# Kernel tuning notes

Hardware: AMD Instinct MI355X
Metric: run time of the kernel (lower is better)

Reference implementation:

```python
import jax, jax.numpy as jnp
import numpy as np

DEPTH, BREADTH, N_HEADS = 6, 1024, 16
D_HEAD = BREADTH // N_HEADS
EPS = 1e-5


def layer_norm(x, g, b):
    m = jnp.mean(x, axis=-1, keepdims=True)
    v = jnp.mean(jnp.square(x - m), axis=-1, keepdims=True)
    return (x - m) * jax.lax.rsqrt(v + EPS) * g + b


def setup_inputs() -> dict:
    key = jax.random.key(0)
    ks = jax.random.split(key, 16)
    B, S, Dm, Dff = 4, 1024, BREADTH, 4 * BREADTH
    s = 0.02
    return {
        "x": jax.random.normal(ks[0], (B, S, Dm), dtype=jnp.float32),
        "mask": jnp.ones((B, S, S), dtype=jnp.int32),
        "wq": s * jax.random.normal(ks[1], (DEPTH, Dm, Dm), dtype=jnp.float32),
        "bq": jnp.zeros((DEPTH, Dm), dtype=jnp.float32),
        "wk": s * jax.random.normal(ks[2], (DEPTH, Dm, Dm), dtype=jnp.float32),
        "bk": jnp.zeros((DEPTH, Dm), dtype=jnp.float32),
        "wv": s * jax.random.normal(ks[3], (DEPTH, Dm, Dm), dtype=jnp.float32),
        "bv": jnp.zeros((DEPTH, Dm), dtype=jnp.float32),
        "wo": s * jax.random.normal(ks[4], (DEPTH, Dm, Dm), dtype=jnp.float32),
        "bo": jnp.zeros((DEPTH, Dm), dtype=jnp.float32),
        "w1": s * jax.random.normal(ks[5], (DEPTH, Dm, Dff), dtype=jnp.float32),
        "b1": jnp.zeros((DEPTH, Dff), dtype=jnp.float32),
        "w2": s * jax.random.normal(ks[6], (DEPTH, Dff, Dm), dtype=jnp.float32),
        "b2": jnp.zeros((DEPTH, Dm), dtype=jnp.float32),
        "ln1g": jnp.ones((DEPTH, Dm), dtype=jnp.float32),
        "ln1b": jnp.zeros((DEPTH, Dm), dtype=jnp.float32),
        "ln2g": jnp.ones((DEPTH, Dm), dtype=jnp.float32),
        "ln2b": jnp.zeros((DEPTH, Dm), dtype=jnp.float32),
        "lnfg": jnp.ones((Dm,), dtype=jnp.float32),
        "lnfb": jnp.zeros((Dm,), dtype=jnp.float32),
    }


def reference(x, mask, wq, bq, wk, bk, wv, bv, wo, bo, w1, b1, w2, b2,
              ln1g, ln1b, ln2g, ln2b, lnfg, lnfb):
    B, S, Dm = x.shape
    scale = 1.0 / jnp.sqrt(jnp.float32(D_HEAD))
    neg = jnp.float32(-1e9)
    mask_b = (mask == 0)[:, None]  # [B,1,S,S]

    def split_heads(t):  # [B,S,Dm] -> [B,H,S,d]
        return t.reshape(B, S, N_HEADS, D_HEAD).transpose(0, 2, 1, 3)

    for i in range(DEPTH):
        xn1 = layer_norm(x, ln1g[i], ln1b[i])  # attention branch input
        xn2 = layer_norm(x, ln2g[i], ln2b[i])  # FFN branch input (pre-attention, per original)

        q = split_heads(xn1 @ wq[i] + bq[i])
        k = split_heads(xn1 @ wk[i] + bk[i])
        v = split_heads(xn1 @ wv[i] + bv[i])
        scores = jnp.einsum("bhqd,bhkd->bhqk", q, k) * scale
        scores = jnp.where(mask_b, neg, scores)
        attn = jax.nn.softmax(scores, axis=-1)
        ctx = jnp.einsum("bhqk,bhkd->bhqd", attn, v)
        ctx = ctx.transpose(0, 2, 1, 3).reshape(B, S, Dm)
        x = x + (ctx @ wo[i] + bo[i])

        h = jax.nn.relu(xn2 @ w1[i] + b1[i])
        x = x + (h @ w2[i] + b2[i])

    return layer_norm(x, lnfg, lnfb)
```

## Files before the change

### kernel.cpp

```cpp
#include <hip/hip_runtime.h>
#include <hip/hip_bf16.h>
#include <stdint.h>

#define DEPTH 6
#define DM 1024
#define DFF 4096
#define NH 16
#define DH 64
#define BATCH 4
#define SEQ 1024
#define NTOK (BATCH*SEQ)
#define QKVLD 3072

using bf16x8 = __attribute__((ext_vector_type(8))) short;
using f32x4  = __attribute__((ext_vector_type(4))) float;
typedef unsigned short u16;

__device__ __forceinline__ u16 f2bf(float f) {
  union { float f; uint32_t u; } v; v.f = f;
  return (u16)((v.u + 0x7FFFu + ((v.u >> 16) & 1u)) >> 16);
}

__device__ __forceinline__ void async16(void* lds, const void* g) {
  __builtin_amdgcn_global_load_lds(
      (__attribute__((address_space(1))) void*)(unsigned long long)g,
      (__attribute__((address_space(3))) void*)(unsigned int)(unsigned long long)lds,
      16, 0, 0);
}

__global__ __launch_bounds__(256)
void prep(const float* __restrict__ wq, const float* __restrict__ wk,
          const float* __restrict__ wv, const float* __restrict__ wo,
          const float* __restrict__ w1, const float* __restrict__ w2,
          const float* __restrict__ bq, const float* __restrict__ bk,
          const float* __restrict__ bv,
          u16* __restrict__ wqkvT, u16* __restrict__ woT,
          u16* __restrict__ w1T, u16* __restrict__ w2T,
          float* __restrict__ bqkv) {
  const int bid = blockIdx.x;
  if (bid >= 12288) {
    const int t = (bid - 12288) * 256 + threadIdx.x;
    bqkv[t] = t < 1024 ? bq[t] : (t < 2048 ? bk[t - 1024] : bv[t - 2048]);
    return;
  }
  const float* w; u16* wt; int K, N, tile;
  if (bid < 3072)      { const int r = bid >> 10;
                         w = r == 0 ? wq : (r == 1 ? wk : wv);
                         wt = wqkvT + (size_t)r * 1024 * 1024; K = 1024; N = 1024; tile = bid & 1023; }
  else if (bid < 4096) { w = wo; wt = woT; K = 1024; N = 1024; tile = bid - 3072; }
  else if (bid < 8192) { w = w1; wt = w1T; K = 1024; N = 4096; tile = bid - 4096; }
  else                 { w = w2; wt = w2T; K = 4096; N = 1024; tile = bid - 8192; }
  const int ntn = N >> 5;
  const int k0 = (tile / ntn) << 5, n0 = (tile % ntn) << 5;

  __shared__ u16 t[32][33];
  const int tx = threadIdx.x & 31, ty = threadIdx.x >> 5;
  #pragma unroll
  for (int r = ty; r < 32; r += 8)
    t[r][tx] = f2bf(w[(size_t)(k0 + r) * N + n0 + tx]);
  __syncthreads();
  #pragma unroll
  for (int r = ty; r < 32; r += 8)
    wt[(size_t)(n0 + r) * K + k0 + tx] = t[tx][r];
}

__global__ __launch_bounds__(256)
void vtrans(const u16* __restrict__ qkv, u16* __restrict__ vt) {
  __shared__ u16 t[64][72];
  const int s0 = blockIdx.x * 64, c0 = blockIdx.y * 64, b = blockIdx.z;
  const int r = threadIdx.x >> 2, cq = threadIdx.x & 3;
  const u16* src = qkv + ((size_t)(b * SEQ + s0 + r)) * QKVLD + 2048 + c0 + cq * 16;
  *(bf16x8*)&t[r][cq * 16]     = *(const bf16x8*)(src);
  *(bf16x8*)&t[r][cq * 16 + 8] = *(const bf16x8*)(src + 8);
  __syncthreads();
  bf16x8 a, bvec;
  #pragma unroll
  for (int i = 0; i < 8; i++) a[i] = (short)t[cq * 16 + i][r];
  #pragma unroll
  for (int i = 0; i < 8; i++) bvec[i] = (short)t[cq * 16 + 8 + i][r];
  u16* dst = vt + ((size_t)(b * 1024 + c0 + r)) * SEQ + s0 + cq * 16;
  *(bf16x8*)dst = a;
  *(bf16x8*)(dst + 8) = bvec;
}

__global__ void flags_init(int* flags) {
  if (threadIdx.x < BATCH) flags[threadIdx.x] = 1;
}
__global__ void mask_flags(const int* __restrict__ mask, int* __restrict__ flags) {
  const size_t n = (size_t)BATCH * SEQ * SEQ;
  for (size_t i = (size_t)blockIdx.x * 256 + threadIdx.x; i < n; i += (size_t)gridDim.x * 256)
    if (mask[i] == 0) flags[i / ((size_t)SEQ * SEQ)] = 0;
}

__global__ __launch_bounds__(256)
void ln_dual(const float* __restrict__ x,
             const float* __restrict__ g1, const float* __restrict__ b1v,
             const float* __restrict__ g2, const float* __restrict__ b2v,
             u16* __restrict__ o1, u16* __restrict__ o2) {
  const int row = blockIdx.x, tid = threadIdx.x;
  const float4 v = ((const float4*)(x + (size_t)row * DM))[tid];
  float s = v.x + v.y + v.z + v.w;
  float sq = v.x*v.x + v.y*v.y + v.z*v.z + v.w*v.w;
  #pragma unroll
  for (int o = 32; o; o >>= 1) { s += __shfl_xor(s, o); sq += __shfl_xor(sq, o); }
  __shared__ float red[8];
  const int lane = tid & 63, w = tid >> 6;
  if (lane == 0) { red[w] = s; red[4 + w] = sq; }
  __syncthreads();
  s = red[0] + red[1] + red[2] + red[3];
  sq = red[4] + red[5] + red[6] + red[7];
  const float mean = s * (1.0f / DM);
  const float rinv = rsqrtf(sq * (1.0f / DM) - mean * mean + 1e-5f);
  const float4 G1 = ((const float4*)g1)[tid], B1 = ((const float4*)b1v)[tid];
  const float4 G2 = ((const float4*)g2)[tid], B2 = ((const float4*)b2v)[tid];
  const float n0 = (v.x - mean) * rinv, n1 = (v.y - mean) * rinv;
  const float n2 = (v.z - mean) * rinv, n3 = (v.w - mean) * rinv;
  ushort4 a, bb;
  a.x = f2bf(n0*G1.x + B1.x); a.y = f2bf(n1*G1.y + B1.y);
  a.z = f2bf(n2*G1.z + B1.z); a.w = f2bf(n3*G1.w + B1.w);
  bb.x = f2bf(n0*G2.x + B2.x); bb.y = f2bf(n1*G2.y + B2.y);
  bb.z = f2bf(n2*G2.z + B2.z); bb.w = f2bf(n3*G2.w + B2.w);
  ((ushort4*)(o1 + (size_t)row * DM))[tid] = a;
  ((ushort4*)(o2 + (size_t)row * DM))[tid] = bb;
}

__global__ __launch_bounds__(256)
void ln_final(const float* __restrict__ x, const float* __restrict__ g,
              const float* __restrict__ b, float* __restrict__ out) {
  const int row = blockIdx.x, tid = threadIdx.x;
  const float4 v = ((const float4*)(x + (size_t)row * DM))[tid];
  float s = v.x + v.y + v.z + v.w;
  float sq = v.x*v.x + v.y*v.y + v.z*v.z + v.w*v.w;
  #pragma unroll
  for (int o = 32; o; o >>= 1) { s += __shfl_xor(s, o); sq += __shfl_xor(sq, o); }
  __shared__ float red[8];
  const int lane = tid & 63, w = tid >> 6;
  if (lane == 0) { red[w] = s; red[4 + w] = sq; }
  __syncthreads();
  s = red[0] + red[1] + red[2] + red[3];
  sq = red[4] + red[5] + red[6] + red[7];
  const float mean = s * (1.0f / DM);
  const float rinv = rsqrtf(sq * (1.0f / DM) - mean * mean + 1e-5f);
  const float4 G = ((const float4*)g)[tid], B = ((const float4*)b)[tid];
  float4 o;
  o.x = (v.x - mean) * rinv * G.x + B.x;
  o.y = (v.y - mean) * rinv * G.y + B.y;
  o.z = (v.z - mean) * rinv * G.z + B.z;
  o.w = (v.w - mean) * rinv * G.w + B.w;
  ((float4*)(out + (size_t)row * DM))[tid] = o;
}

template<int EPI, int BN>
__global__ __launch_bounds__(256)
void gemm_bt(const u16* __restrict__ A, const u16* __restrict__ BT,
             const float* __restrict__ bias,
             u16* __restrict__ Cb, float* __restrict__ Cf,
             int M, int N, int K) {
  constexpr int WCn = BN / 64;
  constexpr int WR  = 4 / WCn;
  constexpr int MF  = 8 / WR;
  constexpr int WRS = 128 / WR;
  __shared__ u16 As[128 * 32];
  __shared__ u16 Bs[BN * 32];
  const int tid = threadIdx.x;
  const int lane = tid & 63, wave = tid >> 6;
  const int wr = wave / WCn, wc = wave % WCn;
  const int l16 = lane & 15, lhi = lane >> 4;

  const int ntn = N / BN;
  const int nwg = (M >> 7) * ntn;
  int wg = (int)blockIdx.x;
  if ((nwg & 7) == 0) { const int q = nwg >> 3; wg = (wg & 7) * q + (wg >> 3); }
  const int tm = wg / ntn, tn = wg % ntn;

  const int srow = tid >> 2, sc = (tid & 3) * 8;
  const u16* Ag0 = A  + (size_t)(tm * 128 + srow) * K + sc;
  const u16* Bg0 = BT + (size_t)(tn * BN + srow) * K + sc;
  const size_t rstep = (size_t)64 * K;
  u16* As0 = As + tid * 8;  u16* As1 = As + 2048 + tid * 8;
  u16* Bs0 = Bs + tid * 8;  u16* Bs1 = Bs + 2048 + tid * 8;

  f32x4 acc[MF][4];
  #pragma unroll
  for (int m = 0; m < MF; m++)
    #pragma unroll
    for (int n = 0; n < 4; n++)
      #pragma unroll
      for (int j = 0; j < 4; j++) acc[m][n][j] = 0.0f;

  for (int k0 = 0; k0 < K; k0 += 32) {
    __syncthreads();
    async16(As0, Ag0 + k0);
    async16(As1, Ag0 + rstep + k0);
    async16(Bs0, Bg0 + k0);
    if constexpr (BN == 128) async16(Bs1, Bg0 + rstep + k0);
    __syncthreads();
    bf16x8 af[MF], bfv[4];
    #pragma unroll
    for (int m = 0; m < MF; m++)
      af[m] = *(const bf16x8*)&As[(wr * WRS + m * 16 + l16) * 32 + lhi * 8];
    #pragma unroll
    for (int n = 0; n < 4; n++)
      bfv[n] = *(const bf16x8*)&Bs[(wc * 64 + n * 16 + l16) * 32 + lhi * 8];
    #pragma unroll
    for (int m = 0; m < MF; m++)
      #pragma unroll
      for (int n = 0; n < 4; n++)
        acc[m][n] = __builtin_amdgcn_mfma_f32_16x16x32_bf16(af[m], bfv[n], acc[m][n], 0, 0, 0);
  }

  const int row0 = tm * 128 + wr * WRS + lhi * 4;
  const int col0 = tn * BN + wc * 64 + l16;
  #pragma unroll
  for (int n = 0; n < 4; n++) {
    const int col = col0 + n * 16;
    const float bv = bias[col];
    #pragma unroll
    for (int m = 0; m < MF; m++) {
      #pragma unroll
      for (int j = 0; j < 4; j++) {
        const int row = row0 + m * 16 + j;
        float v = acc[m][n][j] + bv;
        if constexpr (EPI == 1) v = fmaxf(v, 0.0f);
        if constexpr (EPI <= 1) Cb[(size_t)row * N + col] = f2bf(v);
        else                    Cf[(size_t)row * N + col] += v;
      }
    }
  }
}

__global__ __launch_bounds__(256, 4)
void attn(const u16* __restrict__ QKV, const u16* __restrict__ VTg,
          u16* __restrict__ Octx,
          const int* __restrict__ mask, const int* __restrict__ flags) {
  __shared__ u16 Ks[64 * 64];
  __shared__ u16 VTs[64 * 64];
  __shared__ u16 Ps[4 * 16 * 64];
  const int tid = threadIdx.x, lane = tid & 63, wv = tid >> 6;
  const int l16 = lane & 15, lhi = lane >> 4;
  const int bid = blockIdx.x;
  const int pair = bid >> 4, qblk = bid & 15;
  const int b = pair >> 4, h = pair & 15;
  const int hoff = h * DH;
  const int q0 = qblk * 64 + wv * 16;
  const size_t tokbase = (size_t)b * SEQ;
  const size_t vbase = ((size_t)b * 1024 + hoff) * SEQ;

  bf16x8 qf[2];
  #pragma unroll
  for (int ds = 0; ds < 2; ds++)
    qf[ds] = *(const bf16x8*)&QKV[(tokbase + q0 + l16) * QKVLD + hoff + ds * 32 + lhi * 8];

  f32x4 oacc[4];
  #pragma unroll
  for (int nt = 0; nt < 4; nt++)
    #pragma unroll
    for (int j = 0; j < 4; j++) oacc[nt][j] = 0.0f;
  float mrun = -1e30f, lrun = 0.0f;

  const int allone = flags[b];
  char* PwB = (char*)(Ps + wv * (16 * 64));
  char* KsB = (char*)Ks;
  char* VTB = (char*)VTs;
  const int xw = (l16 & 7) << 4;

  const int srow0 = tid >> 3, scb0 = (tid & 7) ^ (srow0 & 7);
  const int srow1 = (tid + 256) >> 3, scb1 = (tid & 7) ^ (srow1 & 7);
  const int shfl_src = (lane & 48) + ((lane >> 4) << 2);

  for (int kt = 0; kt < SEQ; kt += 64) {
    __syncthreads();
    async16((char*)Ks + tid * 16,
            &QKV[(tokbase + kt + srow0) * QKVLD + 1024 + hoff + scb0 * 8]);
    async16((char*)Ks + 4096 + tid * 16,
            &QKV[(tokbase + kt + srow1) * QKVLD + 1024 + hoff + scb1 * 8]);
    async16((char*)VTs + tid * 16, &VTg[vbase + (size_t)srow0 * SEQ + kt + scb0 * 8]);
    async16((char*)VTs + 4096 + tid * 16, &VTg[vbase + (size_t)srow1 * SEQ + kt + scb1 * 8]);
    __syncthreads();

    f32x4 sacc[4];
    #pragma unroll
    for (int nt = 0; nt < 4; nt++)
      #pragma unroll
      for (int j = 0; j < 4; j++) sacc[nt][j] = 0.0f;
    #pragma unroll
    for (int ds = 0; ds < 2; ds++) {
      bf16x8 kf[4];
      #pragma unroll
      for (int nt = 0; nt < 4; nt++) {
        const int rk = nt * 16 + l16;
        kf[nt] = *(const bf16x8*)(KsB + ((rk * 128 + ds * 64 + lhi * 16) ^ ((rk & 7) << 4)));
      }
      #pragma unroll
      for (int nt = 0; nt < 4; nt++)
        sacc[nt] = __builtin_amdgcn_mfma_f32_16x16x32_bf16(kf[nt], qf[ds], sacc[nt], 0, 0, 0);
    }
    #pragma unroll
    for (int nt = 0; nt < 4; nt++)
      #pragma unroll
      for (int j = 0; j < 4; j++) sacc[nt][j] *= 0.125f;

    if (!allone) {
      const int qg = q0 + l16;
      #pragma unroll
      for (int nt = 0; nt < 4; nt++)
        #pragma unroll
        for (int j = 0; j < 4; j++) {
          const int kc = kt + nt * 16 + lhi * 4 + j;
          if (mask[(tokbase + qg) * SEQ + kc] == 0) sacc[nt][j] = -1e9f;
        }
    }

    float tmax = -1e30f;
    #pragma unroll
    for (int nt = 0; nt < 4; nt++)
      #pragma unroll
      for (int j = 0; j < 4; j++) tmax = fmaxf(tmax, sacc[nt][j]);
    tmax = fmaxf(tmax, __shfl_xor(tmax, 16));
    tmax = fmaxf(tmax, __shfl_xor(tmax, 32));
    const float mnew = fmaxf(mrun, tmax);
    const float corr = __expf(mrun - mnew);
    float p[4][4];
    float tsum = 0.0f;
    #pragma unroll
    for (int nt = 0; nt < 4; nt++)
      #pragma unroll
      for (int j = 0; j < 4; j++) { p[nt][j] = __expf(sacc[nt][j] - mnew); tsum += p[nt][j]; }
    tsum += __shfl_xor(tsum, 16);
    tsum += __shfl_xor(tsum, 32);
    lrun = lrun * corr + tsum;
    mrun = mnew;

    #pragma unroll
    for (int nt = 0; nt < 4; nt++) {
      const uint32_t lo = (uint32_t)f2bf(p[nt][0]) | ((uint32_t)f2bf(p[nt][1]) << 16);
      const uint32_t hi = (uint32_t)f2bf(p[nt][2]) | ((uint32_t)f2bf(p[nt][3]) << 16);
      *(uint64_t*)(PwB + ((l16 * 128 + nt * 32 + lhi * 8) ^ xw)) =
          (uint64_t)lo | ((uint64_t)hi << 32);
    }

    float cj[4];
    #pragma unroll
    for (int j = 0; j < 4; j++) cj[j] = __shfl(corr, shfl_src + j);
    #pragma unroll
    for (int nt = 0; nt < 4; nt++)
      #pragma unroll
      for (int j = 0; j < 4; j++) oacc[nt][j] *= cj[j];

    #pragma unroll
    for (int ksl = 0; ksl < 2; ksl++) {
      const bf16x8 pf = *(const bf16x8*)(PwB + ((l16 * 128 + ksl * 64 + lhi * 16) ^ xw));
      #pragma unroll
      for (int nt = 0; nt < 4; nt++) {
        const int dr = nt * 16 + l16;
        const bf16x8 vf = *(const bf16x8*)(VTB + ((dr * 128 + ksl * 64 + lhi * 16) ^ ((dr & 7) << 4)));
        oacc[nt] = __builtin_amdgcn_mfma_f32_16x16x32_bf16(pf, vf, oacc[nt], 0, 0, 0);
      }
    }
  }

  const float linv = 1.0f / lrun;
  float lj[4];
  #pragma unroll
  for (int j = 0; j < 4; j++) lj[j] = __shfl(linv, shfl_src + j);
  #pragma unroll
  for (int j = 0; j < 4; j++) {
    const size_t rowg = (tokbase + q0 + lhi * 4 + j) * DM + hoff;
    #pragma unroll
    for (int nt = 0; nt < 4; nt++)
      Octx[rowg + nt * 16 + l16] = f2bf(oacc[nt][j] * lj[j]);
  }
}

extern "C" void kernel_launch(void* const* d_in, const int* in_sizes, int n_in,
                              void* d_out, int out_size, void* d_ws, size_t ws_size,
                              hipStream_t stream) {
  const float* x    = (const float*)d_in[0];
  const int*   mask = (const int*)d_in[1];
  const float* wq = (const float*)d_in[2];
  const float* bq = (const float*)d_in[3];
  const float* wk = (const float*)d_in[4];
  const float* bk = (const float*)d_in[5];
  const float* wvp = (const float*)d_in[6];
  const float* bv = (const float*)d_in[7];
  const float* wo = (const float*)d_in[8];
  const float* bo = (const float*)d_in[9];
  const float* w1 = (const float*)d_in[10];
  const float* b1 = (const float*)d_in[11];
  const float* w2 = (const float*)d_in[12];
  const float* b2 = (const float*)d_in[13];
  const float* ln1g = (const float*)d_in[14];
  const float* ln1b = (const float*)d_in[15];
  const float* ln2g = (const float*)d_in[16];
  const float* ln2b = (const float*)d_in[17];
  const float* lnfg = (const float*)d_in[18];
  const float* lnfb = (const float*)d_in[19];

  char* ws = (char*)d_ws;
  float* xbuf = (float*)(ws);
  u16* xn1  = (u16*)(ws + ((size_t)16 << 20));
  u16* xn2  = (u16*)(ws + ((size_t)24 << 20));
  u16* qkv  = (u16*)(ws + ((size_t)32 << 20));
  u16* ctx  = (u16*)(ws + ((size_t)56 << 20));
  u16* hb   = (u16*)(ws + ((size_t)32 << 20));
  u16* wqkvT= (u16*)(ws + ((size_t)64 << 20));
  u16* woT  = (u16*)(ws + ((size_t)70 << 20));
  u16* w1T  = (u16*)(ws + ((size_t)72 << 20));
  u16* w2T  = (u16*)(ws + ((size_t)80 << 20));
  u16* vT   = (u16*)(ws + ((size_t)88 << 20));
  float* bqkv = (float*)(ws + ((size_t)96 << 20));
  int* flags  = (int*)(ws + ((size_t)96 << 20) + 65536);

  hipMemcpyAsync(xbuf, x, (size_t)NTOK * DM * sizeof(float),
                 hipMemcpyDeviceToDevice, stream);
  flags_init<<<1, 64, 0, stream>>>(flags);
  mask_flags<<<1024, 256, 0, stream>>>(mask, flags);

  auto wgs128 = [](int M, int N) { return dim3((unsigned)((M >> 7) * (N >> 7))); };
  auto wgs64  = [](int M, int N) { return dim3((unsigned)((M >> 7) * (N >> 6))); };

  for (int i = 0; i < DEPTH; i++) {
    prep<<<12300, 256, 0, stream>>>(
        wq  + (size_t)i * DM * DM,  wk + (size_t)i * DM * DM,
        wvp + (size_t)i * DM * DM,  wo + (size_t)i * DM * DM,
        w1  + (size_t)i * DM * DFF, w2 + (size_t)i * DFF * DM,
        bq + i * DM, bk + i * DM, bv + i * DM,
        wqkvT, woT, w1T, w2T, bqkv);

    ln_dual<<<NTOK, 256, 0, stream>>>(xbuf, ln1g + i * DM, ln1b + i * DM,
                                      ln2g + i * DM, ln2b + i * DM, xn1, xn2);

    gemm_bt<0, 128><<<wgs128(NTOK, QKVLD), 256, 0, stream>>>(xn1, wqkvT, bqkv, qkv, nullptr,
                                                             NTOK, QKVLD, DM);
    vtrans<<<dim3(16, 16, 4), 256, 0, stream>>>(qkv, vT);

    attn<<<1024, 256, 0, stream>>>(qkv, vT, ctx, mask, flags);

    gemm_bt<2, 64><<<wgs64(NTOK, DM), 256, 0, stream>>>(ctx, woT, bo + i * DM, nullptr, xbuf,
                                                        NTOK, DM, DM);
    gemm_bt<1, 128><<<wgs128(NTOK, DFF), 256, 0, stream>>>(xn2, w1T, b1 + i * DFF, hb, nullptr,
                                                           NTOK, DFF, DM);
    gemm_bt<2, 64><<<wgs64(NTOK, DM), 256, 0, stream>>>(hb, w2T, b2 + i * DM, nullptr, xbuf,
                                                        NTOK, DM, DFF);
  }

  ln_final<<<NTOK, 256, 0, stream>>>(xbuf, lnfg, lnfb, (float*)d_out);
}
```

Before: 1.674 ms.

## Double-buffer LDS tiles in GEMM and attention to overlap loads with MFMA

Both the bf16 GEMM and the flash-attention kernel now keep two LDS buffers and issue the async global-to-LDS loads for the next K tile before computing on the current one, with a single barrier per iteration instead of two. The goal is to hide global memory latency behind MFMA work. This doubles LDS use per block, which may lower occupancy, especially in attention with launch bounds of 4 blocks. The prefetch relies on the trailing barrier to ensure async loads have completed, with no explicit vmcnt wait before reading the other buffer.

```diff
diff --git a/kernel.cpp b/kernel.cpp
--- a/kernel.cpp
+++ b/kernel.cpp
@@ -160,8 +160,10 @@
   constexpr int WR  = 4 / WCn;
   constexpr int MF  = 8 / WR;
   constexpr int WRS = 128 / WR;
-  __shared__ u16 As[128 * 32];
-  __shared__ u16 Bs[BN * 32];
+  constexpr int ASZ = 128 * 32;
+  constexpr int BSZ = BN * 32;
+  __shared__ u16 As[2 * ASZ];
+  __shared__ u16 Bs[2 * BSZ];
   const int tid = threadIdx.x;
   const int lane = tid & 63, wave = tid >> 6;
   const int wr = wave / WCn, wc = wave % WCn;
@@ -177,8 +179,13 @@
   const u16* Ag0 = A  + (size_t)(tm * 128 + srow) * K + sc;
   const u16* Bg0 = BT + (size_t)(tn * BN + srow) * K + sc;
   const size_t rstep = (size_t)64 * K;
-  u16* As0 = As + tid * 8;  u16* As1 = As + 2048 + tid * 8;
-  u16* Bs0 = Bs + tid * 8;  u16* Bs1 = Bs + 2048 + tid * 8;
+
+  auto stage = [&](int buf, int k0) {
+    async16(As + buf * ASZ + tid * 8, Ag0 + k0);
+    async16(As + buf * ASZ + 2048 + tid * 8, Ag0 + rstep + k0);
+    async16(Bs + buf * BSZ + tid * 8, Bg0 + k0);
+    if constexpr (BN == 128) async16(Bs + buf * BSZ + 2048 + tid * 8, Bg0 + rstep + k0);
+  };
 
   f32x4 acc[MF][4];
   #pragma unroll
@@ -188,25 +195,27 @@
       #pragma unroll
       for (int j = 0; j < 4; j++) acc[m][n][j] = 0.0f;
 
+  stage(0, 0);
+  __syncthreads();
+  int cur = 0;
   for (int k0 = 0; k0 < K; k0 += 32) {
-    __syncthreads();
-    async16(As0, Ag0 + k0);
-    async16(As1, Ag0 + rstep + k0);
-    async16(Bs0, Bg0 + k0);
-    if constexpr (BN == 128) async16(Bs1, Bg0 + rstep + k0);
-    __syncthreads();
+    if (k0 + 32 < K) stage(cur ^ 1, k0 + 32);
+    const u16* Ab = As + cur * ASZ;
+    const u16* Bb = Bs + cur * BSZ;
     bf16x8 af[MF], bfv[4];
     #pragma unroll
     for (int m = 0; m < MF; m++)
-      af[m] = *(const bf16x8*)&As[(wr * WRS + m * 16 + l16) * 32 + lhi * 8];
+      af[m] = *(const bf16x8*)&Ab[(wr * WRS + m * 16 + l16) * 32 + lhi * 8];
     #pragma unroll
     for (int n = 0; n < 4; n++)
-      bfv[n] = *(const bf16x8*)&Bs[(wc * 64 + n * 16 + l16) * 32 + lhi * 8];
+      bfv[n] = *(const bf16x8*)&Bb[(wc * 64 + n * 16 + l16) * 32 + lhi * 8];
     #pragma unroll
     for (int m = 0; m < MF; m++)
       #pragma unroll
       for (int n = 0; n < 4; n++)
         acc[m][n] = __builtin_amdgcn_mfma_f32_16x16x32_bf16(af[m], bfv[n], acc[m][n], 0, 0, 0);
+    __syncthreads();
+    cur ^= 1;
   }
 
   const int row0 = tm * 128 + wr * WRS + lhi * 4;
@@ -233,8 +242,8 @@
 void attn(const u16* __restrict__ QKV, const u16* __restrict__ VTg,
           u16* __restrict__ Octx,
           const int* __restrict__ mask, const int* __restrict__ flags) {
-  __shared__ u16 Ks[64 * 64];
-  __shared__ u16 VTs[64 * 64];
+  __shared__ u16 Ks[2 * 64 * 64];
+  __shared__ u16 VTs[2 * 64 * 64];
   __shared__ u16 Ps[4 * 16 * 64];
   const int tid = threadIdx.x, lane = tid & 63, wv = tid >> 6;
   const int l16 = lane & 15, lhi = lane >> 4;
@@ -260,23 +269,30 @@
 
   const int allone = flags[b];
   char* PwB = (char*)(Ps + wv * (16 * 64));
-  char* KsB = (char*)Ks;
-  char* VTB = (char*)VTs;
   const int xw = (l16 & 7) << 4;
 
   const int srow0 = tid >> 3, scb0 = (tid & 7) ^ (srow0 & 7);
   const int srow1 = (tid + 256) >> 3, scb1 = (tid & 7) ^ (srow1 & 7);
   const int shfl_src = (lane & 48) + ((lane >> 4) << 2);
 
+  auto stage = [&](int buf, int kt) {
+    async16((char*)Ks + buf * 8192 + tid * 16,
+            &QKV[(tokbase + kt + srow0) * QKVLD + 1024 + hoff + scb0 * 8]);
+    async16((char*)Ks + buf * 8192 + 4096 + tid * 16,
+            &QKV[(tokbase + kt + srow1) * QKVLD + 1024 + hoff + scb1 * 8]);
+    async16((char*)VTs + buf * 8192 + tid * 16,
+            &VTg[vbase + (size_t)srow0 * SEQ + kt + scb0 * 8]);
+    async16((char*)VTs + buf * 8192 + 4096 + tid * 16,
+            &VTg[vbase + (size_t)srow1 * SEQ + kt + scb1 * 8]);
+  };
+
+  stage(0, 0);
+  __syncthreads();
+  int cur = 0;
   for (int kt = 0; kt < SEQ; kt += 64) {
-    __syncthreads();
-    async16((char*)Ks + tid * 16,
-            &QKV[(tokbase + kt + srow0) * QKVLD + 1024 + hoff + scb0 * 8]);
-    async16((char*)Ks + 4096 + tid * 16,
-            &QKV[(tokbase + kt + srow1) * QKVLD + 1024 + hoff + scb1 * 8]);
-    async16((char*)VTs + tid * 16, &VTg[vbase + (size_t)srow0 * SEQ + kt + scb0 * 8]);
-    async16((char*)VTs + 4096 + tid * 16, &VTg[vbase + (size_t)srow1 * SEQ + kt + scb1 * 8]);
-    __syncthreads();
+    if (kt + 64 < SEQ) stage(cur ^ 1, kt + 64);
+    char* KsB = (char*)Ks + cur * 8192;
+    char* VTB = (char*)VTs + cur * 8192;
 
     f32x4 sacc[4];
     #pragma unroll
@@ -357,6 +373,8 @@
         oacc[nt] = __builtin_amdgcn_mfma_f32_16x16x32_bf16(pf, vf, oacc[nt], 0, 0, 0);
       }
     }
+    __syncthreads();
+    cur ^= 1;
   }
 
   const float linv = 1.0f / lrun;
```

Result: faster. 1.523 ms (-9.0%).
